# Kernel optimization log

Measured on AMD Instinct MI355X. Metric: run time of the kernel, lower is better.

## Reference

```python
import jax, jax.numpy as jnp
import numpy as np

IGNORE_INDEX = -100


def setup_inputs() -> dict:
    key = jax.random.key(0)
    k1, k2, k3 = jax.random.split(key, 3)
    BT, H, V = 4096, 2048, 32000
    hidden_states = jax.random.normal(k1, (BT, H), dtype=jnp.float32) * 0.02
    weight = jax.random.normal(k2, (V, H), dtype=jnp.float32) * 0.02
    targets = jax.random.randint(k3, (BT,), 0, V, dtype=jnp.int64)
    return {"hidden_states": hidden_states, "weight": weight, "targets": targets}


def reference(hidden_states, weight, targets):
    # Fused lm_head projection + cross-entropy with ignore_index masking,
    # 'mean' reduction over valid rows (matches reduction='mean').
    logits = jnp.einsum('bh,vh->bv', hidden_states, weight).astype(jnp.float32)  # (BT, V)
    lse = jax.nn.logsumexp(logits, axis=-1)  # (BT,)
    safe_tgt = jnp.clip(targets, 0, logits.shape[-1] - 1)
    target_logit = jnp.take_along_axis(logits, safe_tgt[:, None], axis=-1)[:, 0]
    valid = targets != IGNORE_INDEX
    loss_rows = jnp.where(valid, lse - target_logit, 0.0)  # (BT,)
    n_valid = jnp.maximum(valid.sum(), 1)
    return loss_rows.sum() / n_valid.astype(jnp.float32)
```

## Files before the change

### kernel.cpp

```cpp
#include <hip/hip_runtime.h>

#define BT 4096
#define H  2048
#define V  32000
#define BM 256
#define BN 256
#define BKB 128
#define KT (H / BKB)
#define NTILES (V / BN)
#define MTILES (BT / BM)
#define NWG (MTILES * NTILES)
#define IGNORE_INDEX (-100)

typedef int   v8i   __attribute__((ext_vector_type(8)));
typedef float f32x4 __attribute__((ext_vector_type(4)));

#define SCALE_ONE 0x7F7F7F7F
#define UNSCALE   (1.0f / 65536.0f)

#define BAR()   __builtin_amdgcn_s_barrier()
#define LGKM0() asm volatile("s_waitcnt lgkmcnt(0)" ::: "memory")
#define LGKM8() asm volatile("s_waitcnt lgkmcnt(8)" ::: "memory")
#define VMC(N)  asm volatile("s_waitcnt vmcnt(" #N ")" ::: "memory")

__device__ inline void load_lds16(const void* g, void* l) {
  __builtin_amdgcn_global_load_lds(
      (const __attribute__((address_space(1))) unsigned int*)g,
      (__attribute__((address_space(3))) unsigned int*)l,
      16, 0, 0);
}

__global__ __launch_bounds__(256)
void cvt_fp8_kernel(const float* __restrict__ in, unsigned int* __restrict__ out, long n8) {
  long i = (long)blockIdx.x * blockDim.x + threadIdx.x;
  long stride = (long)gridDim.x * blockDim.x;
  for (; i < n8; i += stride) {
    float4 x = ((const float4*)in)[2 * i];
    float4 y = ((const float4*)in)[2 * i + 1];
    int lo = 0, hi = 0;
    lo = __builtin_amdgcn_cvt_pk_fp8_f32(x.x * 256.f, x.y * 256.f, lo, false);
    lo = __builtin_amdgcn_cvt_pk_fp8_f32(x.z * 256.f, x.w * 256.f, lo, true);
    hi = __builtin_amdgcn_cvt_pk_fp8_f32(y.x * 256.f, y.y * 256.f, hi, false);
    hi = __builtin_amdgcn_cvt_pk_fp8_f32(y.z * 256.f, y.w * 256.f, hi, true);
    uint2 p; p.x = (unsigned)lo; p.y = (unsigned)hi;
    ((uint2*)out)[i] = p;
  }
}

union frag_u { v8i v; int4 h[2]; };

#define MF(C, A, B)                                                         \
  (C) = __builtin_amdgcn_mfma_scale_f32_16x16x128_f8f6f4(                   \
      (A).v, (B).v, (C), 0, 0, 0, SCALE_ONE, 0, SCALE_ONE)

__global__ __launch_bounds__(512, 2)
void gemm_lse_kernel(const unsigned char* __restrict__ Af8,
                     const unsigned char* __restrict__ Bf8,
                     const int* __restrict__ tgt,
                     float* __restrict__ pm, float* __restrict__ pl,
                     float* __restrict__ tl) {
  __shared__ __align__(16) unsigned char As[2][BM][BKB];
  __shared__ __align__(16) unsigned char Bs[2][BN][BKB];
  __shared__ float red_m[4][BM];
  __shared__ float red_l[4][BM];
  __shared__ int   stgt[BM];

  const int wgid = ((int)blockIdx.x & 7) * (NWG / 8) + ((int)blockIdx.x >> 3);
  const int mt = wgid & (MTILES - 1);
  const int nt = wgid / MTILES;
  const int m0 = mt * BM;
  const int n0 = nt * BN;

  const int tid  = threadIdx.x;
  const int lane = tid & 63;
  const int w    = tid >> 6;
  const int wr   = w >> 2;
  const int wc   = w & 3;
  const int lm   = lane & 15;
  const int q    = lane >> 4;

  if (tid < BM) stgt[tid] = tgt[m0 + tid];
  __syncthreads();

  const int srow = lane >> 3;
  const int gch  = ((lane & 7) ^ srow) * 16;
  const unsigned char* aSrc = Af8 + (size_t)(m0 + w * 16 + srow) * H + gch;
  const unsigned char* bSrc = Bf8 + (size_t)(n0 + w * 16 + srow) * H + gch;

  auto stageA = [&](int buf, int hf, int kt) {
    const unsigned char* s = aSrc + (size_t)hf * 128 * H + (size_t)kt * BKB;
    unsigned char* d = &As[buf][hf * 128 + w * 16][0];
    load_lds16(s, d);
    load_lds16(s + (size_t)8 * H, d + 8 * BKB);
  };
  auto stageB = [&](int buf, int hf, int kt) {
    const unsigned char* s = bSrc + (size_t)hf * 128 * H + (size_t)kt * BKB;
    unsigned char* d = &Bs[buf][hf * 128 + w * 16][0];
    load_lds16(s, d);
    load_lds16(s + (size_t)8 * H, d + 8 * BKB);
  };

  const int c0 = ((2 * q)     ^ (lm & 7)) * 16;
  const int c1 = ((2 * q + 1) ^ (lm & 7)) * 16;
  const unsigned char* aRdB = &As[0][wr * 128 + lm][0];
  const unsigned char* bRdB = &Bs[0][wc * 64 + lm][0];

  auto ldA = [&](frag_u& f, int buf, int ai) {
    const unsigned char* p = aRdB + buf * (BM * BKB) + ai * (16 * BKB);
    f.h[0] = *(const int4*)(p + c0);
    f.h[1] = *(const int4*)(p + c1);
  };
  auto ldB = [&](frag_u& f, int buf, int bj) {
    const unsigned char* p = bRdB + buf * (BN * BKB) + bj * (16 * BKB);
    f.h[0] = *(const int4*)(p + c0);
    f.h[1] = *(const int4*)(p + c1);
  };

  f32x4 acc[8][4];
#pragma unroll
  for (int a = 0; a < 8; ++a)
#pragma unroll
    for (int b = 0; b < 4; ++b) acc[a][b] = (f32x4){0.f, 0.f, 0.f, 0.f};

  frag_u fa0, fa1, fa2, fa3, fb0, fb1, fb2, fb3;

  stageA(0, 0, 0); stageA(0, 1, 0); stageB(0, 0, 0); stageB(0, 1, 0);
  VMC(4);
  stageA(1, 0, 1); stageA(1, 1, 1); stageB(1, 0, 1);
  VMC(6);
  BAR();

  for (int i = 0; i < 8; ++i) {
    const int t0 = 2 * i, t1 = 2 * i + 1;
    const bool pre = (i < 7);

    ldA(fa0, 0, 0); ldA(fa1, 0, 1); ldA(fa2, 0, 2); ldA(fa3, 0, 3);
    ldB(fb0, 0, 0); ldB(fb1, 0, 1);
    stageB(1, 1, t1);
    LGKM8();
    BAR(); LGKM0();
    __builtin_amdgcn_s_setprio(1);
    MF(acc[0][0], fa0, fb0); MF(acc[1][0], fa1, fb0);
    MF(acc[2][0], fa2, fb0); MF(acc[3][0], fa3, fb0);
    MF(acc[0][1], fa0, fb1); MF(acc[1][1], fa1, fb1);
    MF(acc[2][1], fa2, fb1); MF(acc[3][1], fa3, fb1);
    __builtin_amdgcn_s_setprio(0);
    BAR();

    ldB(fb2, 0, 2); ldB(fb3, 0, 3);
    if (pre) stageA(0, 0, t0 + 2);
    BAR(); LGKM0();
    __builtin_amdgcn_s_setprio(1);
    MF(acc[0][2], fa0, fb2); MF(acc[1][2], fa1, fb2);
    MF(acc[2][2], fa2, fb2); MF(acc[3][2], fa3, fb2);
    MF(acc[0][3], fa0, fb3); MF(acc[1][3], fa1, fb3);
    MF(acc[2][3], fa2, fb3); MF(acc[3][3], fa3, fb3);
    __builtin_amdgcn_s_setprio(0);
    BAR();

    ldA(fa0, 0, 4); ldA(fa1, 0, 5); ldA(fa2, 0, 6); ldA(fa3, 0, 7);
    if (pre) stageA(0, 1, t0 + 2);
    BAR(); LGKM0();
    __builtin_amdgcn_s_setprio(1);
    MF(acc[4][0], fa0, fb0); MF(acc[5][0], fa1, fb0);
    MF(acc[6][0], fa2, fb0); MF(acc[7][0], fa3, fb0);
    MF(acc[4][1], fa0, fb1); MF(acc[5][1], fa1, fb1);
    MF(acc[6][1], fa2, fb1); MF(acc[7][1], fa3, fb1);
    __builtin_amdgcn_s_setprio(0);
    BAR();

    if (pre) stageB(0, 0, t0 + 2);
    BAR(); LGKM0();
    __builtin_amdgcn_s_setprio(1);
    MF(acc[4][2], fa0, fb2); MF(acc[5][2], fa1, fb2);
    MF(acc[6][2], fa2, fb2); MF(acc[7][2], fa3, fb2);
    MF(acc[4][3], fa0, fb3); MF(acc[5][3], fa1, fb3);
    MF(acc[6][3], fa2, fb3); MF(acc[7][3], fa3, fb3);
    __builtin_amdgcn_s_setprio(0);
    if (pre) { VMC(6); } else { VMC(0); }
    BAR();

    ldA(fa0, 1, 0); ldA(fa1, 1, 1); ldA(fa2, 1, 2); ldA(fa3, 1, 3);
    ldB(fb0, 1, 0); ldB(fb1, 1, 1);
    if (pre) stageB(0, 1, t0 + 2);
    LGKM8();
    BAR(); LGKM0();
    __builtin_amdgcn_s_setprio(1);
    MF(acc[0][0], fa0, fb0); MF(acc[1][0], fa1, fb0);
    MF(acc[2][0], fa2, fb0); MF(acc[3][0], fa3, fb0);
    MF(acc[0][1], fa0, fb1); MF(acc[1][1], fa1, fb1);
    MF(acc[2][1], fa2, fb1); MF(acc[3][1], fa3, fb1);
    __builtin_amdgcn_s_setprio(0);
    BAR();

    ldB(fb2, 1, 2); ldB(fb3, 1, 3);
    if (pre) stageA(1, 0, t1 + 2);
    BAR(); LGKM0();
    __builtin_amdgcn_s_setprio(1);
    MF(acc[0][2], fa0, fb2); MF(acc[1][2], fa1, fb2);
    MF(acc[2][2], fa2, fb2); MF(acc[3][2], fa3, fb2);
    MF(acc[0][3], fa0, fb3); MF(acc[1][3], fa1, fb3);
    MF(acc[2][3], fa2, fb3); MF(acc[3][3], fa3, fb3);
    __builtin_amdgcn_s_setprio(0);
    BAR();

    ldA(fa0, 1, 4); ldA(fa1, 1, 5); ldA(fa2, 1, 6); ldA(fa3, 1, 7);
    if (pre) stageA(1, 1, t1 + 2);
    BAR(); LGKM0();
    __builtin_amdgcn_s_setprio(1);
    MF(acc[4][0], fa0, fb0); MF(acc[5][0], fa1, fb0);
    MF(acc[6][0], fa2, fb0); MF(acc[7][0], fa3, fb0);
    MF(acc[4][1], fa0, fb1); MF(acc[5][1], fa1, fb1);
    MF(acc[6][1], fa2, fb1); MF(acc[7][1], fa3, fb1);
    __builtin_amdgcn_s_setprio(0);
    BAR();

    if (pre) stageB(1, 0, t1 + 2);
    BAR(); LGKM0();
    __builtin_amdgcn_s_setprio(1);
    MF(acc[4][2], fa0, fb2); MF(acc[5][2], fa1, fb2);
    MF(acc[6][2], fa2, fb2); MF(acc[7][2], fa3, fb2);
    MF(acc[4][3], fa0, fb3); MF(acc[5][3], fa1, fb3);
    MF(acc[6][3], fa2, fb3); MF(acc[7][3], fa3, fb3);
    __builtin_amdgcn_s_setprio(0);
    if (pre) VMC(6);
    BAR();
  }

  __syncthreads();

#pragma unroll
  for (int ai = 0; ai < 8; ++ai) {
#pragma unroll
    for (int r = 0; r < 4; ++r) {
      int row_local = wr * 128 + ai * 16 + q * 4 + r;
      int c = stgt[row_local] - n0 - wc * 64;
      if ((unsigned)c < 64u && (c & 15) == lm) {
        int bj = c >> 4;
        float v = bj == 0 ? acc[ai][0][r]
                : bj == 1 ? acc[ai][1][r]
                : bj == 2 ? acc[ai][2][r]
                :           acc[ai][3][r];
        tl[m0 + row_local] = v * UNSCALE;
      }
    }
  }

#pragma unroll
  for (int ai = 0; ai < 8; ++ai) {
#pragma unroll
    for (int r = 0; r < 4; ++r) {
      float v0 = acc[ai][0][r] * UNSCALE;
      float v1 = acc[ai][1][r] * UNSCALE;
      float v2 = acc[ai][2][r] * UNSCALE;
      float v3 = acc[ai][3][r] * UNSCALE;
      float mx = fmaxf(fmaxf(v0, v1), fmaxf(v2, v3));
#pragma unroll
      for (int off = 1; off < 16; off <<= 1) mx = fmaxf(mx, __shfl_xor(mx, off));
      float s = __expf(v0 - mx) + __expf(v1 - mx) + __expf(v2 - mx) + __expf(v3 - mx);
#pragma unroll
      for (int off = 1; off < 16; off <<= 1) s += __shfl_xor(s, off);
      if (lm == 0) {
        int row_local = wr * 128 + ai * 16 + q * 4 + r;
        red_m[wc][row_local] = mx;
        red_l[wc][row_local] = s;
      }
    }
  }
  __syncthreads();
  if (tid < BM) {
    float M = fmaxf(fmaxf(red_m[0][tid], red_m[1][tid]),
                    fmaxf(red_m[2][tid], red_m[3][tid]));
    float L = red_l[0][tid] * __expf(red_m[0][tid] - M)
            + red_l[1][tid] * __expf(red_m[1][tid] - M)
            + red_l[2][tid] * __expf(red_m[2][tid] - M)
            + red_l[3][tid] * __expf(red_m[3][tid] - M);
    long idx = (long)nt * BT + (m0 + tid);
    pm[idx] = M;
    pl[idx] = L;
  }
}

__global__ __launch_bounds__(256)
void row_lse_kernel(const float* __restrict__ pm, const float* __restrict__ pl,
                    const float* __restrict__ tl, const int* __restrict__ tgt,
                    float* __restrict__ rl) {
  int row  = blockIdx.x * 4 + (threadIdx.x >> 6);
  int lane = threadIdx.x & 63;
  float M = -__builtin_inff();
  float L = 0.f;
  for (int t = lane; t < NTILES; t += 64) {
    float m2 = pm[(long)t * BT + row];
    float l2 = pl[(long)t * BT + row];
    float Mn = fmaxf(M, m2);
    L = L * __expf(M - Mn) + l2 * __expf(m2 - Mn);
    M = Mn;
  }
#pragma unroll
  for (int off = 1; off < 64; off <<= 1) {
    float m2 = __shfl_xor(M, off);
    float l2 = __shfl_xor(L, off);
    float Mn = fmaxf(M, m2);
    L = L * __expf(M - Mn) + l2 * __expf(m2 - Mn);
    M = Mn;
  }
  if (lane == 0) {
    float lse = M + logf(L);
    int t = tgt[row];
    rl[row] = (t != IGNORE_INDEX) ? (lse - tl[row]) : 0.f;
  }
}

__global__ __launch_bounds__(256)
void final_kernel(const float* __restrict__ rl, const int* __restrict__ tgt,
                  float* __restrict__ out) {
  __shared__ float ss[4];
  __shared__ float sc[4];
  float s = 0.f, c = 0.f;
  for (int r = threadIdx.x; r < BT; r += 256) {
    s += rl[r];
    c += (tgt[r] != IGNORE_INDEX) ? 1.f : 0.f;
  }
#pragma unroll
  for (int off = 32; off > 0; off >>= 1) {
    s += __shfl_xor(s, off);
    c += __shfl_xor(c, off);
  }
  int w = threadIdx.x >> 6;
  if ((threadIdx.x & 63) == 0) { ss[w] = s; sc[w] = c; }
  __syncthreads();
  if (threadIdx.x == 0) {
    float S = ss[0] + ss[1] + ss[2] + ss[3];
    float C = sc[0] + sc[1] + sc[2] + sc[3];
    out[0] = S / fmaxf(C, 1.f);
  }
}

extern "C" void kernel_launch(void* const* d_in, const int* in_sizes, int n_in,
                              void* d_out, int out_size, void* d_ws, size_t ws_size,
                              hipStream_t stream) {
  const float* hs  = (const float*)d_in[0];
  const float* wt  = (const float*)d_in[1];
  const int*   tgt = (const int*)d_in[2];
  float*       out = (float*)d_out;

  char* ws = (char*)d_ws;
  size_t off = 0;
  auto alloc = [&](size_t bytes) -> void* {
    void* p = ws + off;
    off += (bytes + 255) & ~(size_t)255;
    return p;
  };
  unsigned char* wf8 = (unsigned char*)alloc((size_t)V * H);
  unsigned char* hf8 = (unsigned char*)alloc((size_t)BT * H);
  float* pm = (float*)alloc((size_t)NTILES * BT * 4);
  float* pl = (float*)alloc((size_t)NTILES * BT * 4);
  float* tl = (float*)alloc((size_t)BT * 4);
  float* rl = (float*)alloc((size_t)BT * 4);
  (void)ws_size; (void)in_sizes; (void)n_in; (void)out_size;

  cvt_fp8_kernel<<<8192, 256, 0, stream>>>(wt, (unsigned int*)wf8, (long)V * H / 8);
  cvt_fp8_kernel<<<1024, 256, 0, stream>>>(hs, (unsigned int*)hf8, (long)BT * H / 8);

  gemm_lse_kernel<<<NWG, 512, 0, stream>>>(hf8, wf8, tgt, pm, pl, tl);

  row_lse_kernel<<<BT / 4, 256, 0, stream>>>(pm, pl, tl, tgt, rl);
  final_kernel<<<1, 256, 0, stream>>>(rl, tgt, out);
}
```

Measured before the change: 763.7 us.

## Store fp8 tiles in fragment-native LDS layout and reorder stage prefetch schedule

```diff
diff --git a/kernel.cpp b/kernel.cpp
--- a/kernel.cpp
+++ b/kernel.cpp
@@ -59,8 +59,8 @@
                      const int* __restrict__ tgt,
                      float* __restrict__ pm, float* __restrict__ pl,
                      float* __restrict__ tl) {
-  __shared__ __align__(16) unsigned char As[2][BM][BKB];
-  __shared__ __align__(16) unsigned char Bs[2][BN][BKB];
+  __shared__ __align__(16) unsigned char As[2 * 32768];
+  __shared__ __align__(16) unsigned char Bs[2 * 32768];
   __shared__ float red_m[4][BM];
   __shared__ float red_l[4][BM];
   __shared__ int   stgt[BM];
@@ -82,38 +82,34 @@
   if (tid < BM) stgt[tid] = tgt[m0 + tid];
   __syncthreads();
 
-  const int srow = lane >> 3;
-  const int gch  = ((lane & 7) ^ srow) * 16;
-  const unsigned char* aSrc = Af8 + (size_t)(m0 + w * 16 + srow) * H + gch;
-  const unsigned char* bSrc = Bf8 + (size_t)(n0 + w * 16 + srow) * H + gch;
+  const unsigned char* aSrc = Af8 + (size_t)(m0 + w * 16 + lm) * H + q * 32;
+  const unsigned char* bSrc = Bf8 + (size_t)(n0 + w * 16 + lm) * H + q * 32;
 
   auto stageA = [&](int buf, int hf, int kt) {
     const unsigned char* s = aSrc + (size_t)hf * 128 * H + (size_t)kt * BKB;
-    unsigned char* d = &As[buf][hf * 128 + w * 16][0];
+    unsigned char* d = As + buf * 32768 + (hf * 8 + w) * 2048;
     load_lds16(s, d);
-    load_lds16(s + (size_t)8 * H, d + 8 * BKB);
+    load_lds16(s + 16, d + 1024);
   };
   auto stageB = [&](int buf, int hf, int kt) {
     const unsigned char* s = bSrc + (size_t)hf * 128 * H + (size_t)kt * BKB;
-    unsigned char* d = &Bs[buf][hf * 128 + w * 16][0];
+    unsigned char* d = Bs + buf * 32768 + (hf * 8 + w) * 2048;
     load_lds16(s, d);
-    load_lds16(s + (size_t)8 * H, d + 8 * BKB);
-  };
-
-  const int c0 = ((2 * q)     ^ (lm & 7)) * 16;
-  const int c1 = ((2 * q + 1) ^ (lm & 7)) * 16;
-  const unsigned char* aRdB = &As[0][wr * 128 + lm][0];
-  const unsigned char* bRdB = &Bs[0][wc * 64 + lm][0];
-
-  auto ldA = [&](frag_u& f, int buf, int ai) {
-    const unsigned char* p = aRdB + buf * (BM * BKB) + ai * (16 * BKB);
-    f.h[0] = *(const int4*)(p + c0);
-    f.h[1] = *(const int4*)(p + c1);
-  };
-  auto ldB = [&](frag_u& f, int buf, int bj) {
-    const unsigned char* p = bRdB + buf * (BN * BKB) + bj * (16 * BKB);
-    f.h[0] = *(const int4*)(p + c0);
-    f.h[1] = *(const int4*)(p + c1);
+    load_lds16(s + 16, d + 1024);
+  };
+
+  const unsigned char* aRd = As + lane * 16;
+  const unsigned char* bRd = Bs + lane * 16;
+
+  auto ldA = [&](frag_u& f, int buf, int i) {
+    const unsigned char* p = aRd + buf * 32768 + (wr * 8 + i) * 2048;
+    f.h[0] = *(const int4*)(p);
+    f.h[1] = *(const int4*)(p + 1024);
+  };
+  auto ldB = [&](frag_u& f, int buf, int j) {
+    const unsigned char* p = bRd + buf * 32768 + (wc * 4 + j) * 2048;
+    f.h[0] = *(const int4*)(p);
+    f.h[1] = *(const int4*)(p + 1024);
   };
 
   f32x4 acc[8][4];
@@ -125,9 +121,8 @@
   frag_u fa0, fa1, fa2, fa3, fb0, fb1, fb2, fb3;
 
   stageA(0, 0, 0); stageA(0, 1, 0); stageB(0, 0, 0); stageB(0, 1, 0);
+  stageB(1, 0, 1); stageB(1, 1, 1);
   VMC(4);
-  stageA(1, 0, 1); stageA(1, 1, 1); stageB(1, 0, 1);
-  VMC(6);
   BAR();
 
   for (int i = 0; i < 8; ++i) {
@@ -136,7 +131,7 @@
 
     ldA(fa0, 0, 0); ldA(fa1, 0, 1); ldA(fa2, 0, 2); ldA(fa3, 0, 3);
     ldB(fb0, 0, 0); ldB(fb1, 0, 1);
-    stageB(1, 1, t1);
+    stageA(1, 0, t1);
     LGKM8();
     BAR(); LGKM0();
     __builtin_amdgcn_s_setprio(1);
@@ -148,7 +143,7 @@
     BAR();
 
     ldB(fb2, 0, 2); ldB(fb3, 0, 3);
-    if (pre) stageA(0, 0, t0 + 2);
+    stageA(1, 1, t1);
     BAR(); LGKM0();
     __builtin_amdgcn_s_setprio(1);
     MF(acc[0][2], fa0, fb2); MF(acc[1][2], fa1, fb2);
@@ -159,7 +154,7 @@
     BAR();
 
     ldA(fa0, 0, 4); ldA(fa1, 0, 5); ldA(fa2, 0, 6); ldA(fa3, 0, 7);
-    if (pre) stageA(0, 1, t0 + 2);
+    if (pre) stageB(0, 0, t0 + 2);
     BAR(); LGKM0();
     __builtin_amdgcn_s_setprio(1);
     MF(acc[4][0], fa0, fb0); MF(acc[5][0], fa1, fb0);
@@ -169,7 +164,7 @@
     __builtin_amdgcn_s_setprio(0);
     BAR();
 
-    if (pre) stageB(0, 0, t0 + 2);
+    if (pre) stageB(0, 1, t0 + 2);
     BAR(); LGKM0();
     __builtin_amdgcn_s_setprio(1);
     MF(acc[4][2], fa0, fb2); MF(acc[5][2], fa1, fb2);
@@ -177,12 +172,12 @@
     MF(acc[4][3], fa0, fb3); MF(acc[5][3], fa1, fb3);
     MF(acc[6][3], fa2, fb3); MF(acc[7][3], fa3, fb3);
     __builtin_amdgcn_s_setprio(0);
-    if (pre) { VMC(6); } else { VMC(0); }
+    if (pre) { VMC(4); } else { VMC(0); }
     BAR();
 
     ldA(fa0, 1, 0); ldA(fa1, 1, 1); ldA(fa2, 1, 2); ldA(fa3, 1, 3);
     ldB(fb0, 1, 0); ldB(fb1, 1, 1);
-    if (pre) stageB(0, 1, t0 + 2);
+    if (pre) stageA(0, 0, t0 + 2);
     LGKM8();
     BAR(); LGKM0();
     __builtin_amdgcn_s_setprio(1);
@@ -194,7 +189,7 @@
     BAR();
 
     ldB(fb2, 1, 2); ldB(fb3, 1, 3);
-    if (pre) stageA(1, 0, t1 + 2);
+    if (pre) stageA(0, 1, t0 + 2);
     BAR(); LGKM0();
     __builtin_amdgcn_s_setprio(1);
     MF(acc[0][2], fa0, fb2); MF(acc[1][2], fa1, fb2);
@@ -205,7 +200,7 @@
     BAR();
 
     ldA(fa0, 1, 4); ldA(fa1, 1, 5); ldA(fa2, 1, 6); ldA(fa3, 1, 7);
-    if (pre) stageA(1, 1, t1 + 2);
+    if (pre) stageB(1, 0, t1 + 2);
     BAR(); LGKM0();
     __builtin_amdgcn_s_setprio(1);
     MF(acc[4][0], fa0, fb0); MF(acc[5][0], fa1, fb0);
@@ -215,7 +210,7 @@
     __builtin_amdgcn_s_setprio(0);
     BAR();
 
-    if (pre) stageB(1, 0, t1 + 2);
+    if (pre) stageB(1, 1, t1 + 2);
     BAR(); LGKM0();
     __builtin_amdgcn_s_setprio(1);
     MF(acc[4][2], fa0, fb2); MF(acc[5][2], fa1, fb2);
@@ -223,7 +218,7 @@
     MF(acc[4][3], fa0, fb3); MF(acc[5][3], fa1, fb3);
     MF(acc[6][3], fa2, fb3); MF(acc[7][3], fa3, fb3);
     __builtin_amdgcn_s_setprio(0);
-    if (pre) VMC(6);
+    if (pre) { VMC(4); } else { VMC(0); }
     BAR();
   }
 
```

New measurement: 832.9 us. 9.1% more time.
